# Kernel tuning notes

Measured on AMD Instinct MI355X. Metric: run time of the kernel, lower is better.

The kernel has to match this reference:

```python
import jax, jax.numpy as jnp
import numpy as np

# static config (matches init_kwargs)
IMAGE_SIZE = 224
PATCH = 16
DIM = 768
DEPTH = 12
HEADS = 12
HEAD_DIM = DIM // HEADS
MLP_DIM = int(DIM * 4.0)
N_CLASSES = 1000
BATCH = 32
MASK = (True, False, True, False, True, False, True, False, True, False, True, False)
SCALE = HEAD_DIM ** -0.5
LN_EPS = 1e-5


def setup_inputs() -> dict:
    key = jax.random.key(0)
    ks = jax.random.split(key, 20)
    std = 0.02
    d = {}
    d['x'] = jax.random.normal(ks[0], (BATCH, 3, IMAGE_SIZE, IMAGE_SIZE), jnp.float32)
    patch_dim = 3 * PATCH * PATCH
    d['patch_w'] = jax.random.normal(ks[1], (DIM, patch_dim), jnp.float32) * std
    d['patch_b'] = jnp.zeros((DIM,), jnp.float32)
    d['cls_token'] = jax.random.normal(ks[2], (1, 1, DIM), jnp.float32) * std
    n_tok = (IMAGE_SIZE // PATCH) ** 2 + 1
    d['pos_embed'] = jax.random.normal(ks[3], (1, n_tok, DIM), jnp.float32) * std
    # stacked per-layer params (torch Linear convention: [out, in])
    d['ln1_w'] = jnp.ones((DEPTH, DIM), jnp.float32)
    d['ln1_b'] = jnp.zeros((DEPTH, DIM), jnp.float32)
    d['qkv_w'] = jax.random.normal(ks[4], (DEPTH, 3 * DIM, DIM), jnp.float32) * std
    d['proj_w'] = jax.random.normal(ks[5], (DEPTH, DIM, DIM), jnp.float32) * std
    d['proj_b'] = jnp.zeros((DEPTH, DIM), jnp.float32)
    d['ln2_w'] = jnp.ones((DEPTH, DIM), jnp.float32)
    d['ln2_b'] = jnp.zeros((DEPTH, DIM), jnp.float32)
    d['mlp_w1'] = jax.random.normal(ks[6], (DEPTH, MLP_DIM, DIM), jnp.float32) * std
    d['mlp_b1'] = jnp.zeros((DEPTH, MLP_DIM), jnp.float32)
    d['mlp_w2'] = jax.random.normal(ks[7], (DEPTH, DIM, MLP_DIM), jnp.float32) * std
    d['mlp_b2'] = jnp.zeros((DEPTH, DIM), jnp.float32)
    # L2Q polynomial params, 'quadratic' init mode (only used where MASK[i])
    d['alpha'] = jnp.full((DEPTH, HEADS), 0.125, jnp.float32)
    d['beta'] = jnp.full((DEPTH, HEADS), 0.5, jnp.float32)
    d['gamma'] = jnp.zeros((DEPTH, HEADS), jnp.float32)
    d['norm_w'] = jnp.ones((DIM,), jnp.float32)
    d['norm_b'] = jnp.zeros((DIM,), jnp.float32)
    d['head_w'] = jax.random.normal(ks[8], (N_CLASSES, DIM), jnp.float32) * std
    d['head_b'] = jnp.zeros((N_CLASSES,), jnp.float32)
    return d


def _ln(x, w, b):
    mu = x.mean(-1, keepdims=True)
    var = ((x - mu) ** 2).mean(-1, keepdims=True)
    return (x - mu) * jax.lax.rsqrt(var + LN_EPS) * w + b


def _patchify(x):
    B, C, H, W = x.shape
    p = PATCH
    x = x.reshape(B, C, H // p, p, W // p, p)
    x = x.transpose(0, 2, 4, 1, 3, 5)
    return x.reshape(B, (H // p) * (W // p), C * p * p)


def _vit_forward(x, patch_w, patch_b, cls_token, pos_embed, ln1_w, ln1_b,
                 qkv_w, proj_w, proj_b, ln2_w, ln2_b,
                 mlp_w1, mlp_b1, mlp_w2, mlp_b2,
                 alpha, beta, gamma, norm_w, norm_b, head_w, head_b):
    B = x.shape[0]
    tok = _patchify(x) @ patch_w.T + patch_b          # [B, N-1, D]
    cls = jnp.broadcast_to(cls_token, (B, 1, DIM))
    h = jnp.concatenate([cls, tok], axis=1) + pos_embed  # [B, N, D]
    N = h.shape[1]
    for i in range(DEPTH):
        # --- attention ---
        a_in = _ln(h, ln1_w[i], ln1_b[i])
        qkv = a_in @ qkv_w[i].T                        # [B, N, 3D]
        qkv = qkv.reshape(B, N, 3, HEADS, HEAD_DIM).transpose(2, 0, 3, 1, 4)
        q, k, v = qkv[0], qkv[1], qkv[2]               # [B, H, N, hd]
        logits = jnp.einsum('bhnd,bhmd->bhnm', q, k) * SCALE
        if MASK[i]:  # L2Q polynomial attention
            a = alpha[i][None, :, None, None]
            b_ = beta[i][None, :, None, None]
            g = gamma[i][None, :, None, None]
            attn = jax.nn.relu(a * logits * logits + b_ * logits + g)
            attn = attn / (attn.sum(-1, keepdims=True) + 1e-6)
        else:        # standard softmax attention
            attn = jax.nn.softmax(logits, axis=-1)
        o = jnp.einsum('bhnm,bhmd->bhnd', attn, v)
        o = o.transpose(0, 2, 1, 3).reshape(B, N, DIM)
        h = h + o @ proj_w[i].T + proj_b[i]
        # --- MLP ---
        m_in = _ln(h, ln2_w[i], ln2_b[i])
        m = jax.nn.gelu(m_in @ mlp_w1[i].T + mlp_b1[i], approximate=False)
        h = h + m @ mlp_w2[i].T + mlp_b2[i]
    cls_out = _ln(h[:, 0], norm_w, norm_b)
    return cls_out @ head_w.T + head_b                 # [B, n_classes]


def reference(x, patch_w, patch_b, cls_token, pos_embed, ln1_w, ln1_b,
              qkv_w, proj_w, proj_b, ln2_w, ln2_b,
              mlp_w1, mlp_b1, mlp_w2, mlp_b2,
              alpha, beta, gamma, norm_w, norm_b, head_w, head_b):
    return _vit_forward(x, patch_w, patch_b, cls_token, pos_embed, ln1_w, ln1_b,
                        qkv_w, proj_w, proj_b, ln2_w, ln2_b,
                        mlp_w1, mlp_b1, mlp_w2, mlp_b2,
                        alpha, beta, gamma, norm_w, norm_b, head_w, head_b)
```

## Files before the change

### kernel.cpp

```cpp
#include <hip/hip_runtime.h>
#include <math.h>

#define B_    32
#define NT    197
#define NP    196
#define D_    768
#define NH    12
#define HD_   64
#define MLP_  3072
#define QKVD  2304
#define NCLS  1000

typedef unsigned short u16;
typedef __bf16 bf16x8 __attribute__((ext_vector_type(8)));
typedef float  f32x4  __attribute__((ext_vector_type(4)));
struct alignas(8) u16x4_t { u16 x, y, z, w; };

__device__ __forceinline__ u16 f2bf(float f) {
    unsigned u = __builtin_bit_cast(unsigned, f);
    u = u + 0x7FFFu + ((u >> 16) & 1u);
    return (u16)(u >> 16);
}
__device__ __forceinline__ void gload_lds16(const void* g, void* l) {
    __builtin_amdgcn_global_load_lds((const __attribute__((address_space(1))) unsigned*)g,
                                     (__attribute__((address_space(3))) unsigned*)l, 16, 0, 0);
}
__device__ __forceinline__ float gelu_f(float x) {
    float u = 0.7978845608f * (x + 0.044715f * x * x * x);
    u = fminf(fmaxf(u, -10.f), 10.f);
    float e = __expf(2.f * u);
    float t = (e - 1.f) * __builtin_amdgcn_rcpf(e + 1.f);
    return 0.5f * x * (1.f + t);
}

__global__ void patchify_k(const float* __restrict__ x, u16* __restrict__ tok) {
    int bp = blockIdx.x;
    int b = bp / NP, p = bp % NP;
    int ph = p / 14, pw = p % 14;
    const float* xb = x + (size_t)b * 3 * 224 * 224;
    u16* trow = tok + (size_t)bp * D_;
    for (int f = threadIdx.x; f < D_; f += blockDim.x) {
        int c = f >> 8;
        int r = f & 255;
        int i = r >> 4, j = r & 15;
        trow[f] = f2bf(xb[((size_t)c * 224 + (ph * 16 + i)) * 224 + (pw * 16 + j)]);
    }
}

__global__ void assemble_h_k(const float* __restrict__ tokemb, const float* __restrict__ cls,
                             const float* __restrict__ pos, float* __restrict__ h) {
    int bn = blockIdx.x;
    int b = bn / NT, n = bn % NT;
    float* hr = h + (size_t)bn * D_;
    const float* pr = pos + (size_t)n * D_;
    if (n == 0) {
        for (int d = threadIdx.x; d < D_; d += blockDim.x) hr[d] = cls[d] + pr[d];
    } else {
        const float* tr = tokemb + ((size_t)b * NP + (n - 1)) * D_;
        for (int d = threadIdx.x; d < D_; d += blockDim.x) hr[d] = tr[d] + pr[d];
    }
}

__global__ void cvt1_k(const float* __restrict__ src, u16* __restrict__ dst, int n4) {
    int i = (blockIdx.x * 256 + threadIdx.x) * 4;
    if (i >= n4) return;
    float4 v = *(const float4*)(src + i);
    u16x4_t o; o.x = f2bf(v.x); o.y = f2bf(v.y); o.z = f2bf(v.z); o.w = f2bf(v.w);
    *(u16x4_t*)(dst + i) = o;
}

__global__ void cvtw_k(const float* __restrict__ qw, const float* __restrict__ pw,
                       const float* __restrict__ m1, const float* __restrict__ m2,
                       u16* __restrict__ dst) {
    const size_t n0 = 1769472, n1 = 2359296, n2 = 4718592, n3 = 7077888;
    size_t e = ((size_t)blockIdx.x * 256 + threadIdx.x) * 4;
    if (e >= n3) return;
    const float* src; size_t off;
    if (e < n0)      { src = qw; off = e; }
    else if (e < n1) { src = pw; off = e - n0; }
    else if (e < n2) { src = m1; off = e - n1; }
    else             { src = m2; off = e - n2; }
    float4 v = *(const float4*)(src + off);
    u16x4_t o; o.x = f2bf(v.x); o.y = f2bf(v.y); o.z = f2bf(v.z); o.w = f2bf(v.w);
    *(u16x4_t*)(dst + e) = o;
}

template<int OUTBF>
__global__ __launch_bounds__(256) void ln_k(const float* __restrict__ in, size_t in_row_stride,
                                            const float* __restrict__ w, const float* __restrict__ b,
                                            float* __restrict__ of, u16* __restrict__ ob) {
    int row = blockIdx.x;
    const float* xr = in + (size_t)row * in_row_stride;
    int tid = threadIdx.x;
    float s1 = 0.f, s2 = 0.f;
    for (int d = tid; d < D_; d += 256) { float v = xr[d]; s1 += v; s2 += v * v; }
    #pragma unroll
    for (int off = 32; off; off >>= 1) { s1 += __shfl_down(s1, off); s2 += __shfl_down(s2, off); }
    __shared__ float r1[4], r2[4];
    int wave = tid >> 6, lane = tid & 63;
    if (lane == 0) { r1[wave] = s1; r2[wave] = s2; }
    __syncthreads();
    float m1 = (r1[0] + r1[1] + r1[2] + r1[3]) * (1.0f / D_);
    float m2 = (r2[0] + r2[1] + r2[2] + r2[3]) * (1.0f / D_);
    float rs = rsqrtf(m2 - m1 * m1 + 1e-5f);
    for (int d = tid; d < D_; d += 256) {
        float y = (xr[d] - m1) * rs * w[d] + b[d];
        if (OUTBF) ob[(size_t)row * D_ + d] = f2bf(y);
        else       of[(size_t)row * D_ + d] = y;
    }
}

template<int EPI>
__global__ __launch_bounds__(256) void mgemm_k(const u16* __restrict__ A, const u16* __restrict__ W,
                                               const float* __restrict__ bias, float* __restrict__ Cf,
                                               u16* __restrict__ Cb, int M, int N, int K) {
    __shared__ u16 As[128 * 64];
    __shared__ u16 Ws[128 * 64];
    const int tid = threadIdx.x;
    const int lane = tid & 63, wv = tid >> 6;
    const int wr = wv >> 1, wc = wv & 1;
    const int bm = blockIdx.y * 128, bn = blockIdx.x * 128;
    const int rloc = tid >> 3;
    const int cs8 = ((tid & 7) ^ (rloc & 7)) * 8;
    const int l15 = lane & 15, quad = lane >> 4;
    const int sw = l15 & 7;
    f32x4 acc[4][4] = {};
    for (int k0 = 0; k0 < K; k0 += 64) {
        #pragma unroll
        for (int q = 0; q < 4; ++q) {
            int gr = bm + q * 32 + rloc;
            if (gr > M - 1) gr = M - 1;
            gload_lds16(A + (size_t)gr * K + k0 + cs8, (char*)As + q * 4096 + tid * 16);
        }
        #pragma unroll
        for (int q = 0; q < 4; ++q) {
            int r = q * 32 + rloc;
            gload_lds16(W + (size_t)(bn + r) * K + k0 + cs8, (char*)Ws + q * 4096 + tid * 16);
        }
        __syncthreads();
        #pragma unroll
        for (int kk = 0; kk < 64; kk += 32) {
            const int kc = (kk >> 3) + quad;
            const int co = ((kc ^ sw) * 8);
            bf16x8 af[4], bfr[4];
            #pragma unroll
            for (int i = 0; i < 4; ++i)
                af[i] = *(const bf16x8*)(As + (wr * 64 + i * 16 + l15) * 64 + co);
            #pragma unroll
            for (int j = 0; j < 4; ++j)
                bfr[j] = *(const bf16x8*)(Ws + (wc * 64 + j * 16 + l15) * 64 + co);
            #pragma unroll
            for (int i = 0; i < 4; ++i)
                #pragma unroll
                for (int j = 0; j < 4; ++j)
                    acc[i][j] = __builtin_amdgcn_mfma_f32_16x16x32_bf16(af[i], bfr[j], acc[i][j], 0, 0, 0);
        }
        __syncthreads();
    }
    #pragma unroll
    for (int i = 0; i < 4; ++i) {
        int rb = bm + wr * 64 + i * 16 + quad * 4;
        #pragma unroll
        for (int j = 0; j < 4; ++j) {
            int gc = bn + wc * 64 + j * 16 + l15;
            #pragma unroll
            for (int r = 0; r < 4; ++r) {
                int gr = rb + r;
                if (gr >= M) continue;
                float v = acc[i][j][r];
                if (bias) v += bias[gc];
                size_t idx = (size_t)gr * N + gc;
                if (EPI == 0)      Cf[idx] = v;
                else if (EPI == 1) Cf[idx] += v;
                else if (EPI == 3) Cb[idx] = f2bf(v);
                else Cb[idx] = f2bf(gelu_f(v));
            }
        }
    }
}

__global__ __launch_bounds__(256) void head_k(const float* __restrict__ A, const float* __restrict__ W,
                                              const float* __restrict__ bias, float* __restrict__ C) {
    const int c = blockIdx.x * 4 + (threadIdx.x >> 6);
    const int lane = threadIdx.x & 63;
    const float* wr = W + (size_t)c * D_;
    float acc[32];
    #pragma unroll
    for (int r = 0; r < 32; ++r) acc[r] = 0.f;
    #pragma unroll
    for (int i = 0; i < 12; ++i) {
        float wv = wr[lane + 64 * i];
        #pragma unroll
        for (int r = 0; r < 32; ++r)
            acc[r] = fmaf(A[r * D_ + lane + 64 * i], wv, acc[r]);
    }
    #pragma unroll
    for (int r = 0; r < 32; ++r) {
        #pragma unroll
        for (int off = 32; off; off >>= 1) acc[r] += __shfl_xor(acc[r], off);
    }
    if (lane == 0) {
        const float bb = bias[c];
        #pragma unroll
        for (int r = 0; r < 32; ++r) C[(size_t)r * NCLS + c] = acc[r] + bb;
    }
}

__global__ __launch_bounds__(256) void attn_k(const u16* __restrict__ qkv, u16* __restrict__ o,
                                              const float* __restrict__ alpha, const float* __restrict__ beta,
                                              const float* __restrict__ gamma, int layer, int poly) {
    __shared__ u16 Kb[208 * 72];
    __shared__ u16 Vt[64 * 232];
    __shared__ u16 Pb[4][16 * 40];
    const int tid = threadIdx.x, wv = tid >> 6, lane = tid & 63;
    const int l15 = lane & 15, quad = lane >> 4;
    const int id = blockIdx.x;
    const int half = id & 1, bh = id >> 1;
    const int hh = bh % NH, b = bh / NH;
    const u16* base = qkv + (size_t)b * NT * QKVD;
    for (int idx = tid; idx < 208 * 64; idx += 256) {
        int m = idx >> 6, d = idx & 63;
        Kb[m * 72 + d] = (m < NT) ? base[(size_t)m * QKVD + D_ + hh * 64 + d] : (u16)0;
    }
    for (int idx = tid; idx < 224 * 64; idx += 256) {
        int m = idx >> 6, d = idx & 63;
        Vt[d * 232 + m] = (m < NT) ? base[(size_t)m * QKVD + 2 * D_ + hh * 64 + d] : (u16)0;
    }
    __syncthreads();
    float pa = 0.f, pcb = 0.f, pg = 0.f;
    if (poly) { pa = alpha[layer * NH + hh]; pcb = beta[layer * NH + hh]; pg = gamma[layer * NH + hh]; }

    for (int qt = half + 2 * wv; qt < 13; qt += 8) {
        int qrow = qt * 16 + l15; if (qrow > NT - 1) qrow = NT - 1;
        const u16* qp = base + (size_t)qrow * QKVD + hh * 64;
        bf16x8 aq0 = *(const bf16x8*)(qp + quad * 8);
        bf16x8 aq1 = *(const bf16x8*)(qp + 32 + quad * 8);
        f32x4 S[13];
        #pragma unroll
        for (int f = 0; f < 13; ++f) {
            const u16* kp = Kb + (f * 16 + l15) * 72;
            bf16x8 b0 = *(const bf16x8*)(kp + quad * 8);
            bf16x8 b1 = *(const bf16x8*)(kp + 32 + quad * 8);
            f32x4 c = {};
            c = __builtin_amdgcn_mfma_f32_16x16x32_bf16(aq0, b0, c, 0, 0, 0);
            c = __builtin_amdgcn_mfma_f32_16x16x32_bf16(aq1, b1, c, 0, 0, 0);
            S[f] = c;
        }
        float inv[4];
        if (poly) {
            float s[4] = {0.f, 0.f, 0.f, 0.f};
            #pragma unroll
            for (int f = 0; f < 13; ++f) {
                bool iv = (f == 12) && (l15 >= 5);
                #pragma unroll
                for (int r = 0; r < 4; ++r) {
                    float l = S[f][r] * 0.125f;
                    float p = fmaxf(pa * l * l + pcb * l + pg, 0.f);
                    if (iv) p = 0.f;
                    S[f][r] = p;
                    s[r] += p;
                }
            }
            #pragma unroll
            for (int off = 1; off < 16; off <<= 1)
                #pragma unroll
                for (int r = 0; r < 4; ++r) s[r] += __shfl_xor(s[r], off);
            #pragma unroll
            for (int r = 0; r < 4; ++r) inv[r] = 1.f / (s[r] + 1e-6f);
        } else {
            float mx[4] = {-1e30f, -1e30f, -1e30f, -1e30f};
            #pragma unroll
            for (int f = 0; f < 13; ++f) {
                bool iv = (f == 12) && (l15 >= 5);
                #pragma unroll
                for (int r = 0; r < 4; ++r) {
                    float l = iv ? -1e30f : S[f][r] * 0.125f;
                    S[f][r] = l;
                    mx[r] = fmaxf(mx[r], l);
                }
            }
            #pragma unroll
            for (int off = 1; off < 16; off <<= 1)
                #pragma unroll
                for (int r = 0; r < 4; ++r) mx[r] = fmaxf(mx[r], __shfl_xor(mx[r], off));
            float s[4] = {0.f, 0.f, 0.f, 0.f};
            #pragma unroll
            for (int f = 0; f < 13; ++f)
                #pragma unroll
                for (int r = 0; r < 4; ++r) {
                    float e = __expf(S[f][r] - mx[r]);
                    S[f][r] = e;
                    s[r] += e;
                }
            #pragma unroll
            for (int off = 1; off < 16; off <<= 1)
                #pragma unroll
                for (int r = 0; r < 4; ++r) s[r] += __shfl_xor(s[r], off);
            #pragma unroll
            for (int r = 0; r < 4; ++r) inv[r] = 1.f / s[r];
        }
        #pragma unroll
        for (int f = 0; f < 13; ++f)
            #pragma unroll
            for (int r = 0; r < 4; ++r) S[f][r] *= inv[r];
        f32x4 O[4] = {};
        u16* pb = &Pb[wv][0];
        #pragma unroll
        for (int c = 0; c < 7; ++c) {
            int f0 = 2 * c, f1 = 2 * c + 1;
            __asm__ volatile("s_waitcnt lgkmcnt(0)" ::: "memory");
            #pragma unroll
            for (int r = 0; r < 4; ++r) {
                pb[(quad * 4 + r) * 40 + l15]      = f2bf(S[f0][r]);
                pb[(quad * 4 + r) * 40 + 16 + l15] = (f1 < 13) ? f2bf(S[f1][r]) : (u16)0;
            }
            __asm__ volatile("s_waitcnt lgkmcnt(0)" ::: "memory");
            bf16x8 ap = *(const bf16x8*)(pb + l15 * 40 + quad * 8);
            #pragma unroll
            for (int dt = 0; dt < 4; ++dt) {
                bf16x8 bv = *(const bf16x8*)(Vt + (dt * 16 + l15) * 232 + c * 32 + quad * 8);
                O[dt] = __builtin_amdgcn_mfma_f32_16x16x32_bf16(ap, bv, O[dt], 0, 0, 0);
            }
        }
        #pragma unroll
        for (int dt = 0; dt < 4; ++dt)
            #pragma unroll
            for (int r = 0; r < 4; ++r) {
                int n = qt * 16 + quad * 4 + r;
                if (n < NT)
                    o[((size_t)b * NT + n) * D_ + hh * 64 + dt * 16 + l15] = f2bf(O[dt][r]);
            }
    }
}

extern "C" void kernel_launch(void* const* d_in, const int* in_sizes, int n_in,
                              void* d_out, int out_size, void* d_ws, size_t ws_size,
                              hipStream_t stream) {
    (void)in_sizes; (void)n_in; (void)out_size; (void)ws_size;
    const float* x        = (const float*)d_in[0];
    const float* patch_w  = (const float*)d_in[1];
    const float* patch_b  = (const float*)d_in[2];
    const float* cls_tok  = (const float*)d_in[3];
    const float* pos      = (const float*)d_in[4];
    const float* ln1_w    = (const float*)d_in[5];
    const float* ln1_b    = (const float*)d_in[6];
    const float* qkv_w    = (const float*)d_in[7];
    const float* proj_w   = (const float*)d_in[8];
    const float* proj_b   = (const float*)d_in[9];
    const float* ln2_w    = (const float*)d_in[10];
    const float* ln2_b    = (const float*)d_in[11];
    const float* mlp_w1   = (const float*)d_in[12];
    const float* mlp_b1   = (const float*)d_in[13];
    const float* mlp_w2   = (const float*)d_in[14];
    const float* mlp_b2   = (const float*)d_in[15];
    const float* alpha    = (const float*)d_in[16];
    const float* beta     = (const float*)d_in[17];
    const float* gamma    = (const float*)d_in[18];
    const float* norm_w   = (const float*)d_in[19];
    const float* norm_b   = (const float*)d_in[20];
    const float* head_w   = (const float*)d_in[21];
    const float* head_b   = (const float*)d_in[22];

    const int MASK[12] = {1,0,1,0,1,0,1,0,1,0,1,0};
    const size_t ROWS = (size_t)B_ * NT;

    char* p = (char*)d_ws;
    float* h    = (float*)p;  p += ROWS * D_ * 4;
    float* qkvb = (float*)p;  p += ROWS * QKVD * 4;
    u16*   abuf = (u16*)p;    p += ROWS * D_ * 2;
    u16*   gbuf = (u16*)p;    p += ROWS * MLP_ * 2;
    u16*   wbuf = (u16*)p;    p += (size_t)7077888 * 2;
    float* hb   = (float*)p;  p += 32 * D_ * 4;
    u16*   qkvbf = (u16*)qkvb;

    u16* wq = wbuf;
    u16* wp = wq + 1769472;
    u16* w1 = wp + 589824;
    u16* w2 = w1 + 2359296;

    cvt1_k<<<576, 256, 0, stream>>>(patch_w, wbuf, 589824);
    patchify_k<<<B_ * NP, 256, 0, stream>>>(x, gbuf);
    mgemm_k<0><<<dim3(D_ / 128, 49), 256, 0, stream>>>(gbuf, wbuf, patch_b, qkvb, nullptr,
                                                       B_ * NP, D_, D_);
    assemble_h_k<<<B_ * NT, 256, 0, stream>>>(qkvb, cls_tok, pos, h);

    for (int i = 0; i < 12; ++i) {
        cvtw_k<<<6912, 256, 0, stream>>>(qkv_w + (size_t)i * 1769472, proj_w + (size_t)i * 589824,
                                         mlp_w1 + (size_t)i * 2359296, mlp_w2 + (size_t)i * 2359296, wbuf);
        ln_k<1><<<(int)ROWS, 256, 0, stream>>>(h, D_, ln1_w + (size_t)i * D_, ln1_b + (size_t)i * D_,
                                               nullptr, abuf);
        mgemm_k<3><<<dim3(QKVD / 128, 50), 256, 0, stream>>>(abuf, wq, nullptr, nullptr, qkvbf,
                                                             (int)ROWS, QKVD, D_);
        attn_k<<<B_ * NH * 2, 256, 0, stream>>>(qkvbf, abuf, alpha, beta, gamma, i, MASK[i]);
        mgemm_k<1><<<dim3(D_ / 128, 50), 256, 0, stream>>>(abuf, wp, proj_b + (size_t)i * D_, h, nullptr,
                                                           (int)ROWS, D_, D_);
        ln_k<1><<<(int)ROWS, 256, 0, stream>>>(h, D_, ln2_w + (size_t)i * D_, ln2_b + (size_t)i * D_,
                                               nullptr, abuf);
        mgemm_k<2><<<dim3(MLP_ / 128, 50), 256, 0, stream>>>(abuf, w1, mlp_b1 + (size_t)i * MLP_,
                                                             nullptr, gbuf, (int)ROWS, MLP_, D_);
        mgemm_k<1><<<dim3(D_ / 128, 50), 256, 0, stream>>>(gbuf, w2, mlp_b2 + (size_t)i * D_, h, nullptr,
                                                           (int)ROWS, D_, MLP_);
    }

    ln_k<0><<<B_, 256, 0, stream>>>(h, (size_t)NT * D_, norm_w, norm_b, hb, nullptr);
    head_k<<<250, 256, 0, stream>>>(hb, head_w, head_b, (float*)d_out);
}
```

Before: 4.960 ms.

## Double-buffer GEMM LDS tiles and remap workgroups for XCD-aware locality

The bf16 MFMA GEMM now keeps two LDS buffers and issues the global-to-LDS loads for the next K tile before computing the current one, with one barrier per iteration instead of two. Launches switch to a 1D grid, and block indices are remapped so that consecutive tiles land on the same XCD, which should improve L2 reuse of the shared A and W tiles. LDS use doubles to 64KB per block, which may reduce occupancy. The single barrier must still order correctly against the asynchronous LDS loads into the buffer being overwritten.

After: 4.642 ms. 6.4% less time.

```diff
diff --git a/kernel.cpp b/kernel.cpp
--- a/kernel.cpp
+++ b/kernel.cpp
@@ -113,31 +113,45 @@
 template<int EPI>
 __global__ __launch_bounds__(256) void mgemm_k(const u16* __restrict__ A, const u16* __restrict__ W,
                                                const float* __restrict__ bias, float* __restrict__ Cf,
-                                               u16* __restrict__ Cb, int M, int N, int K) {
-    __shared__ u16 As[128 * 64];
-    __shared__ u16 Ws[128 * 64];
+                                               u16* __restrict__ Cb, int M, int N, int K, int nbn) {
+    __shared__ u16 As[2][128 * 64];
+    __shared__ u16 Ws[2][128 * 64];
     const int tid = threadIdx.x;
     const int lane = tid & 63, wv = tid >> 6;
     const int wr = wv >> 1, wc = wv & 1;
-    const int bm = blockIdx.y * 128, bn = blockIdx.x * 128;
+    const int nwg = gridDim.x;
+    const int orig = blockIdx.x;
+    const int xcd = orig & 7;
+    const int qq = nwg >> 3, rr = nwg & 7;
+    const int lin = (xcd < rr ? xcd * (qq + 1) : rr * (qq + 1) + (xcd - rr) * qq) + (orig >> 3);
+    const int bm = (lin / nbn) * 128, bn = (lin % nbn) * 128;
     const int rloc = tid >> 3;
     const int cs8 = ((tid & 7) ^ (rloc & 7)) * 8;
     const int l15 = lane & 15, quad = lane >> 4;
     const int sw = l15 & 7;
     f32x4 acc[4][4] = {};
-    for (int k0 = 0; k0 < K; k0 += 64) {
+
+    auto stage = [&](int sel, int k0) {
         #pragma unroll
         for (int q = 0; q < 4; ++q) {
             int gr = bm + q * 32 + rloc;
             if (gr > M - 1) gr = M - 1;
-            gload_lds16(A + (size_t)gr * K + k0 + cs8, (char*)As + q * 4096 + tid * 16);
+            gload_lds16(A + (size_t)gr * K + k0 + cs8, (char*)As[sel] + q * 4096 + tid * 16);
         }
         #pragma unroll
         for (int q = 0; q < 4; ++q) {
             int r = q * 32 + rloc;
-            gload_lds16(W + (size_t)(bn + r) * K + k0 + cs8, (char*)Ws + q * 4096 + tid * 16);
-        }
+            gload_lds16(W + (size_t)(bn + r) * K + k0 + cs8, (char*)Ws[sel] + q * 4096 + tid * 16);
+        }
+    };
+
+    const int nk = K >> 6;
+    stage(0, 0);
+    for (int t = 0; t < nk; ++t) {
         __syncthreads();
+        if (t + 1 < nk) stage((t + 1) & 1, (t + 1) << 6);
+        const u16* Asb = As[t & 1];
+        const u16* Wsb = Ws[t & 1];
         #pragma unroll
         for (int kk = 0; kk < 64; kk += 32) {
             const int kc = (kk >> 3) + quad;
@@ -145,17 +159,16 @@
             bf16x8 af[4], bfr[4];
             #pragma unroll
             for (int i = 0; i < 4; ++i)
-                af[i] = *(const bf16x8*)(As + (wr * 64 + i * 16 + l15) * 64 + co);
+                af[i] = *(const bf16x8*)(Asb + (wr * 64 + i * 16 + l15) * 64 + co);
             #pragma unroll
             for (int j = 0; j < 4; ++j)
-                bfr[j] = *(const bf16x8*)(Ws + (wc * 64 + j * 16 + l15) * 64 + co);
+                bfr[j] = *(const bf16x8*)(Wsb + (wc * 64 + j * 16 + l15) * 64 + co);
             #pragma unroll
             for (int i = 0; i < 4; ++i)
                 #pragma unroll
                 for (int j = 0; j < 4; ++j)
                     acc[i][j] = __builtin_amdgcn_mfma_f32_16x16x32_bf16(af[i], bfr[j], acc[i][j], 0, 0, 0);
         }
-        __syncthreads();
     }
     #pragma unroll
     for (int i = 0; i < 4; ++i) {
@@ -380,8 +393,8 @@
 
     cvt1_k<<<576, 256, 0, stream>>>(patch_w, wbuf, 589824);
     patchify_k<<<B_ * NP, 256, 0, stream>>>(x, gbuf);
-    mgemm_k<0><<<dim3(D_ / 128, 49), 256, 0, stream>>>(gbuf, wbuf, patch_b, qkvb, nullptr,
-                                                       B_ * NP, D_, D_);
+    mgemm_k<0><<<6 * 49, 256, 0, stream>>>(gbuf, wbuf, patch_b, qkvb, nullptr,
+                                           B_ * NP, D_, D_, 6);
     assemble_h_k<<<B_ * NT, 256, 0, stream>>>(qkvb, cls_tok, pos, h);
 
     for (int i = 0; i < 12; ++i) {
@@ -389,17 +402,17 @@
                                          mlp_w1 + (size_t)i * 2359296, mlp_w2 + (size_t)i * 2359296, wbuf);
         ln_k<1><<<(int)ROWS, 256, 0, stream>>>(h, D_, ln1_w + (size_t)i * D_, ln1_b + (size_t)i * D_,
                                                nullptr, abuf);
-        mgemm_k<3><<<dim3(QKVD / 128, 50), 256, 0, stream>>>(abuf, wq, nullptr, nullptr, qkvbf,
-                                                             (int)ROWS, QKVD, D_);
+        mgemm_k<3><<<18 * 50, 256, 0, stream>>>(abuf, wq, nullptr, nullptr, qkvbf,
+                                                (int)ROWS, QKVD, D_, 18);
         attn_k<<<B_ * NH * 2, 256, 0, stream>>>(qkvbf, abuf, alpha, beta, gamma, i, MASK[i]);
-        mgemm_k<1><<<dim3(D_ / 128, 50), 256, 0, stream>>>(abuf, wp, proj_b + (size_t)i * D_, h, nullptr,
-                                                           (int)ROWS, D_, D_);
+        mgemm_k<1><<<6 * 50, 256, 0, stream>>>(abuf, wp, proj_b + (size_t)i * D_, h, nullptr,
+                                               (int)ROWS, D_, D_, 6);
         ln_k<1><<<(int)ROWS, 256, 0, stream>>>(h, D_, ln2_w + (size_t)i * D_, ln2_b + (size_t)i * D_,
                                                nullptr, abuf);
-        mgemm_k<2><<<dim3(MLP_ / 128, 50), 256, 0, stream>>>(abuf, w1, mlp_b1 + (size_t)i * MLP_,
-                                                             nullptr, gbuf, (int)ROWS, MLP_, D_);
-        mgemm_k<1><<<dim3(D_ / 128, 50), 256, 0, stream>>>(gbuf, w2, mlp_b2 + (size_t)i * D_, h, nullptr,
-                                                           (int)ROWS, D_, MLP_);
+        mgemm_k<2><<<24 * 50, 256, 0, stream>>>(abuf, w1, mlp_b1 + (size_t)i * MLP_,
+                                                nullptr, gbuf, (int)ROWS, MLP_, D_, 24);
+        mgemm_k<1><<<6 * 50, 256, 0, stream>>>(gbuf, w2, mlp_b2 + (size_t)i * D_, h, nullptr,
+                                               (int)ROWS, D_, MLP_, 6);
     }
 
     ln_k<0><<<B_, 256, 0, stream>>>(h, (size_t)NT * D_, norm_w, norm_b, hb, nullptr);
```
